# Performance work log

Measured on AMD Instinct MI355X. Metric: run time of the kernel, lower is better.

Reference implementation:

```python
import jax, jax.numpy as jnp
import numpy as np

E_DIM = 640   # RNA-FM embedding dim
H = 256       # hidden_dim
L = 3         # num_gcn_layers
LN_EPS = 1e-5


def _layer_norm(x, g, b):
    mu = jnp.mean(x, axis=-1, keepdims=True)
    var = jnp.mean((x - mu) ** 2, axis=-1, keepdims=True)
    return (x - mu) * jax.lax.rsqrt(var + LN_EPS) * g + b


def setup_inputs() -> dict:
    key = jax.random.key(0)
    ks = jax.random.split(key, 20)
    B, S = 4, 256

    def w(k, shape):
        fan_in = shape[-2] if len(shape) >= 2 else shape[-1]
        return jax.random.normal(k, shape, dtype=jnp.float32) / np.sqrt(fan_in)

    inp = {
        "embeddings": jax.random.normal(ks[0], (B, S, E_DIM), dtype=jnp.float32),
        "bp_priors": jax.random.uniform(ks[1], (B, S, S), dtype=jnp.float32),
        "sequence_lengths": jnp.full((B,), S, dtype=jnp.int32),
        # FeatureEncoder: Linear(640, 512) -> ReLU -> Linear(512, 256)
        "enc_w1": w(ks[2], (E_DIM, 2 * H)), "enc_b1": jnp.zeros((2 * H,), jnp.float32),
        "enc_w2": w(ks[3], (2 * H, H)),     "enc_b2": jnp.zeros((H,), jnp.float32),
        # GCN layers (stacked over L)
        "gcn_wself": w(ks[4], (L, H, H)), "gcn_bself": jnp.zeros((L, H), jnp.float32),
        "gcn_wedge": w(ks[5], (L, H, H)), "gcn_bedge": jnp.zeros((L, H), jnp.float32),
        "gcn_ln_g": jnp.ones((L, H), jnp.float32), "gcn_ln_b": jnp.zeros((L, H), jnp.float32),
        # PairwiseScorer MLP: Linear(2H+1, H) -> ReLU -> Linear(H, H//2) -> ReLU -> Linear(H//2, 1)
        "mlp_w1": w(ks[6], (2 * H + 1, H)), "mlp_b1": jnp.zeros((H,), jnp.float32),
        "mlp_w2": w(ks[7], (H, H // 2)),    "mlp_b2": jnp.zeros((H // 2,), jnp.float32),
        "mlp_w3": w(ks[8], (H // 2, 1)),    "mlp_b3": jnp.zeros((1,), jnp.float32),
    }
    return inp


def reference(embeddings, bp_priors, sequence_lengths,
              enc_w1, enc_b1, enc_w2, enc_b2,
              gcn_wself, gcn_bself, gcn_wedge, gcn_bedge, gcn_ln_g, gcn_ln_b,
              mlp_w1, mlp_b1, mlp_w2, mlp_b2, mlp_w3, mlp_b3):
    # FeatureEncoder
    h = jax.nn.relu(embeddings @ enc_w1 + enc_b1) @ enc_w2 + enc_b2  # [B,S,H]

    # GCN layers: self GEMM + adjacency (bp_priors) aggregated neighbor GEMM
    for l in range(L):
        self_f = h @ gcn_wself[l] + gcn_bself[l]
        neigh_f = jnp.einsum('bij,bjh->bih', bp_priors, h @ gcn_wedge[l] + gcn_bedge[l])
        h = _layer_norm(jax.nn.relu(self_f + neigh_f), gcn_ln_g[l], gcn_ln_b[l])

    # PairwiseScorer: concat([node_i, node_j, prior]) @ W1 split into three partial products
    # (mathematically identical to the expand-concat-MLP in the torch module).
    hi = h @ mlp_w1[:H]           # [B,S,H] contribution of node_i
    hj = h @ mlp_w1[H:2 * H]      # [B,S,H] contribution of node_j
    p = jax.nn.relu(hi[:, :, None, :] + hj[:, None, :, :]
                    + bp_priors[..., None] * mlp_w1[2 * H] + mlp_b1)  # [B,S,S,H]
    p = jax.nn.relu(p @ mlp_w2 + mlp_b2)                              # [B,S,S,H//2]
    bp_scores = (p @ mlp_w3 + mlp_b3)[..., 0]                         # [B,S,S]
    return bp_scores
```

## Files before the change

### kernel.cpp

```cpp
#include <hip/hip_runtime.h>

typedef __attribute__((ext_vector_type(8))) short short8;
typedef __attribute__((ext_vector_type(4))) float f32x4;
typedef __attribute__((ext_vector_type(4))) unsigned uint4v;

__device__ __forceinline__ void gload_lds16(const void* g, void* l) {
    __builtin_amdgcn_global_load_lds(
        (const __attribute__((address_space(1))) unsigned*)g,
        (__attribute__((address_space(3))) unsigned*)l, 16, 0, 0);
}
#define MFMA16(a, b, c) __builtin_amdgcn_mfma_f32_16x16x32_bf16((a), (b), (c), 0, 0, 0)

template<bool RELU, bool LNA, bool SPLITW2>
__global__ __launch_bounds__(256)
void gemm_s(const float* __restrict__ A,
            const float* __restrict__ B0, const float* __restrict__ bias0,
            float* __restrict__ C0,
            const float* __restrict__ B1, const float* __restrict__ bias1,
            float* __restrict__ C1,
            const float* __restrict__ ps, const float* __restrict__ lg,
            const float* __restrict__ lb,
            int M, int N, int K, int nxHalf,
            const float* __restrict__ w2, short* __restrict__ w2th,
            short* __restrict__ w2tl)
{
    if (SPLITW2 && blockIdx.y >= 32) {
        int e = ((blockIdx.y - 32) * gridDim.x + blockIdx.x) * 256 + threadIdx.x;
        if (e < 32768) {
            int k = e >> 7, n = e & 127;
            float x = w2[e];
            unsigned hu = __float_as_uint(x) & 0xFFFF0000u;
            w2th[n * 256 + k] = (short)(hu >> 16);
            w2tl[n * 256 + k] = (short)(__float_as_uint(x - __uint_as_float(hu)) >> 16);
        }
        return;
    }
    int bx = blockIdx.x;
    const float* B = B0; const float* bias = bias0; float* C = C0;
    if (nxHalf && bx >= nxHalf) { bx -= nxHalf; B = B1; bias = bias1; C = C1; }
    const int m0 = blockIdx.y * 32, n0 = bx * 32;
    const int tid = threadIdx.x;
    const int tx = tid & 7, ty = tid >> 3;

    __shared__ __align__(16) float As[32 * 36];
    __shared__ __align__(16) float Bs[32 * 36];
    __shared__ float mus[32], rss[32];

    if (LNA) {
        if (tid < 32) {
            int m = m0 + tid;
            float s  = ps[m * 2]            + ps[2048 + m * 2]
                     + ps[4096 + m * 2]     + ps[6144 + m * 2];
            float s2 = ps[m * 2 + 1]        + ps[2048 + m * 2 + 1]
                     + ps[4096 + m * 2 + 1] + ps[6144 + m * 2 + 1];
            float mu  = s * (1.f / 256.f);
            float var = s2 * (1.f / 256.f) - mu * mu;
            mus[tid] = mu;
            rss[tid] = rsqrtf(var + 1e-5f);
        }
        __syncthreads();
    }

    float acc[4] = {};
    for (int k0 = 0; k0 < K; k0 += 32) {
        {
            int row = ty, kq = tx << 2;
            float4 v = *(const float4*)&A[(long)(m0 + row) * K + k0 + kq];
            if (LNA) {
                float4 gv = *(const float4*)&lg[k0 + kq];
                float4 bv = *(const float4*)&lb[k0 + kq];
                float mu = mus[row], rs = rss[row];
                v.x = (v.x - mu) * rs * gv.x + bv.x;
                v.y = (v.y - mu) * rs * gv.y + bv.y;
                v.z = (v.z - mu) * rs * gv.z + bv.z;
                v.w = (v.w - mu) * rs * gv.w + bv.w;
            }
            As[(kq + 0) * 36 + row] = v.x; As[(kq + 1) * 36 + row] = v.y;
            As[(kq + 2) * 36 + row] = v.z; As[(kq + 3) * 36 + row] = v.w;
        }
        *(float4*)&Bs[ty * 36 + tx * 4] =
            *(const float4*)&B[(long)(k0 + ty) * N + n0 + tx * 4];
        __syncthreads();
#pragma unroll
        for (int k = 0; k < 32; ++k) {
            float a = As[k * 36 + ty];
            float4 b4 = *(const float4*)&Bs[k * 36 + tx * 4];
            acc[0] += a * b4.x; acc[1] += a * b4.y;
            acc[2] += a * b4.z; acc[3] += a * b4.w;
        }
        __syncthreads();
    }

    int m = m0 + ty;
#pragma unroll
    for (int j = 0; j < 4; ++j) {
        int n = n0 + tx * 4 + j;
        float v = acc[j];
        if (bias) v += bias[n];
        if (RELU) v = fmaxf(v, 0.f);
        C[(long)m * N + n] = v;
    }
}

__global__ __launch_bounds__(256)
void bmm_fuse(const float* __restrict__ bp, const float* __restrict__ eg,
              const float* __restrict__ sf, float* __restrict__ x,
              float* __restrict__ ps)
{
    const int b = blockIdx.z, jb = blockIdx.x;
    const int m0 = blockIdx.y * 32, n0 = jb * 64;
    const float* A = bp + b * 65536;
    const float* B = eg + b * 65536;
    const int tid = threadIdx.x;
    const int tx = tid & 15, ty = tid >> 4;

    __shared__ __align__(16) float As[32 * 36];
    __shared__ __align__(16) float Bs[32 * 68];

    float acc[2][4] = {};
    for (int k0 = 0; k0 < 256; k0 += 32) {
        {
            int row = tid >> 3, kq = (tid & 7) << 2;
            float4 v = *(const float4*)&A[(long)(m0 + row) * 256 + k0 + kq];
            As[(kq + 0) * 36 + row] = v.x; As[(kq + 1) * 36 + row] = v.y;
            As[(kq + 2) * 36 + row] = v.z; As[(kq + 3) * 36 + row] = v.w;
        }
#pragma unroll
        for (int q = 0; q < 2; ++q) {
            int f = tid * 2 + q;
            int kk = f >> 4, nn = (f & 15) << 2;
            *(float4*)&Bs[kk * 68 + nn] = *(const float4*)&B[(long)(k0 + kk) * 256 + n0 + nn];
        }
        __syncthreads();
#pragma unroll
        for (int k = 0; k < 32; ++k) {
            float2 a2 = *(const float2*)&As[k * 36 + ty * 2];
            float4 b4 = *(const float4*)&Bs[k * 68 + tx * 4];
            acc[0][0] += a2.x * b4.x; acc[0][1] += a2.x * b4.y;
            acc[0][2] += a2.x * b4.z; acc[0][3] += a2.x * b4.w;
            acc[1][0] += a2.y * b4.x; acc[1][1] += a2.y * b4.y;
            acc[1][2] += a2.y * b4.z; acc[1][3] += a2.y * b4.w;
        }
        __syncthreads();
    }

#pragma unroll
    for (int i = 0; i < 2; ++i) {
        int gm = b * 256 + m0 + ty * 2 + i;
        float s = 0.f, s2 = 0.f;
#pragma unroll
        for (int j = 0; j < 4; ++j) {
            int n = n0 + tx * 4 + j;
            float v = fmaxf(acc[i][j] + sf[(long)gm * 256 + n], 0.f);
            x[(long)gm * 256 + n] = v;
            s += v; s2 += v * v;
        }
        s  += __shfl_xor(s, 1, 64);  s2 += __shfl_xor(s2, 1, 64);
        s  += __shfl_xor(s, 2, 64);  s2 += __shfl_xor(s2, 2, 64);
        s  += __shfl_xor(s, 4, 64);  s2 += __shfl_xor(s2, 4, 64);
        s  += __shfl_xor(s, 8, 64);  s2 += __shfl_xor(s2, 8, 64);
        if (tx == 0) {
            ps[jb * 2048 + gm * 2]     = s;
            ps[jb * 2048 + gm * 2 + 1] = s2;
        }
    }
}

#define STAGE_HJ(T, BUF)                                                        \
    {                                                                           \
        int row = tid >> 3, s = tid & 7;                                        \
        gload_lds16(&hja[((long)(b * 256 + j0 + row)) * 256 + (T) * 32          \
                         + ((s ^ (row & 7)) << 2)],                             \
                    (char*)&hjs[BUF][0] + tid * 16);                            \
        int row2 = row + 32;                                                    \
        gload_lds16(&hja[((long)(b * 256 + j0 + row2)) * 256 + (T) * 32         \
                         + ((s ^ (row2 & 7)) << 2)],                            \
                    (char*)&hjs[BUF][0] + 4096 + tid * 16);                     \
    }

#define BUILD_P(KT, BUF)                                                        \
    {                                                                           \
        const char* hbase = (const char*)&hjs[BUF][0] + jj * 128;               \
        char* phc = (char*)&Ph[BUF][0];                                         \
        char* plc = (char*)&Pl[BUF][0];                                         \
        const int swz = (p & 7) << 4;                                           \
        _Pragma("unroll")                                                       \
        for (int q = 0; q < 2; ++q) {                                           \
            const int oct = o0 + q;                                             \
            float4 hv0 = *(const float4*)(hbase + (((oct * 2)     ^ (jj & 7)) << 4)); \
            float4 hv1 = *(const float4*)(hbase + (((oct * 2 + 1) ^ (jj & 7)) << 4)); \
            float4 iv0 = *(const float4*)&hib[ii][(KT) * 32 + oct * 8];         \
            float4 iv1 = *(const float4*)&hib[ii][(KT) * 32 + oct * 8 + 4];     \
            float4 cv0 = *(const float4*)&csv[(KT) * 32 + oct * 8];             \
            float4 cv1 = *(const float4*)&csv[(KT) * 32 + oct * 8 + 4];         \
            float x0 = fmaxf(fmaf(bpw, cv0.x, iv0.x) + hv0.x, 0.f);             \
            float x1 = fmaxf(fmaf(bpw, cv0.y, iv0.y) + hv0.y, 0.f);             \
            float x2 = fmaxf(fmaf(bpw, cv0.z, iv0.z) + hv0.z, 0.f);             \
            float x3 = fmaxf(fmaf(bpw, cv0.w, iv0.w) + hv0.w, 0.f);             \
            float x4 = fmaxf(fmaf(bpw, cv1.x, iv1.x) + hv1.x, 0.f);             \
            float x5 = fmaxf(fmaf(bpw, cv1.y, iv1.y) + hv1.y, 0.f);             \
            float x6 = fmaxf(fmaf(bpw, cv1.z, iv1.z) + hv1.z, 0.f);             \
            float x7 = fmaxf(fmaf(bpw, cv1.w, iv1.w) + hv1.w, 0.f);             \
            unsigned h0 = __float_as_uint(x0) & 0xFFFF0000u;                    \
            unsigned h1 = __float_as_uint(x1) & 0xFFFF0000u;                    \
            unsigned h2 = __float_as_uint(x2) & 0xFFFF0000u;                    \
            unsigned h3 = __float_as_uint(x3) & 0xFFFF0000u;                    \
            unsigned h4 = __float_as_uint(x4) & 0xFFFF0000u;                    \
            unsigned h5 = __float_as_uint(x5) & 0xFFFF0000u;                    \
            unsigned h6 = __float_as_uint(x6) & 0xFFFF0000u;                    \
            unsigned h7 = __float_as_uint(x7) & 0xFFFF0000u;                    \
            uint4v hv_, lv_;                                                    \
            hv_[0] = (h0 >> 16) | h1;                                           \
            hv_[1] = (h2 >> 16) | h3;                                           \
            hv_[2] = (h4 >> 16) | h5;                                           \
            hv_[3] = (h6 >> 16) | h7;                                           \
            lv_[0] = (__float_as_uint(x0 - __uint_as_float(h0)) >> 16)          \
                   | (__float_as_uint(x1 - __uint_as_float(h1)) & 0xFFFF0000u); \
            lv_[1] = (__float_as_uint(x2 - __uint_as_float(h2)) >> 16)          \
                   | (__float_as_uint(x3 - __uint_as_float(h3)) & 0xFFFF0000u); \
            lv_[2] = (__float_as_uint(x4 - __uint_as_float(h4)) >> 16)          \
                   | (__float_as_uint(x5 - __uint_as_float(h5)) & 0xFFFF0000u); \
            lv_[3] = (__float_as_uint(x6 - __uint_as_float(h6)) >> 16)          \
                   | (__float_as_uint(x7 - __uint_as_float(h7)) & 0xFFFF0000u); \
            int sbyte = p * 64 + oct * 16;                                      \
            *(uint4v*)(phc + (sbyte ^ swz)) = hv_;                              \
            *(uint4v*)(plc + (sbyte ^ swz)) = lv_;                              \
        }                                                                       \
    }

__global__ __launch_bounds__(256, 3)
void pairwise4(const float* __restrict__ hia, const float* __restrict__ hja,
               const float* __restrict__ bpm,
               const float* __restrict__ c, const float* __restrict__ b1,
               const short* __restrict__ w2th, const short* __restrict__ w2tl,
               const float* __restrict__ b2, const float* __restrict__ w3,
               const float* __restrict__ b3, float* __restrict__ out)
{
    const int b = blockIdx.z, ib0 = blockIdx.y * 2, j0 = blockIdx.x * 64;
    const int tid = threadIdx.x, l = tid & 63, wid = tid >> 6;
    const int wm0 = (wid & 1) * 64, wn0 = (wid >> 1) * 64;
    const int g = l >> 4, ln = l & 15;
    const int p = tid >> 1, jj = p & 63, ii = p >> 6, o0 = (tid & 1) * 2;

    __shared__ __align__(16) short Ph[2][4096];
    __shared__ __align__(16) short Pl[2][4096];
    __shared__ __align__(16) float hjs[2][2048];
    __shared__ __align__(16) float hib[2][256];
    __shared__ __align__(16) float csv[256];
    __shared__ float bpv[128];
    __shared__ float red[128][2];

    if (tid < 128)
        bpv[tid] = bpm[((long)(b * 256 + ib0 + (tid >> 6))) * 256 + j0 + (tid & 63)];
    {
        int i2 = tid >> 7, kk = (tid & 127) * 2;
        float2 hv = *(const float2*)&hia[((long)(b * 256 + ib0 + i2)) * 256 + kk];
        float2 bv = *(const float2*)&b1[kk];
        hib[i2][kk] = hv.x + bv.x; hib[i2][kk + 1] = hv.y + bv.y;
    }
    if (tid < 64) *(float4*)&csv[tid * 4] = *(const float4*)&c[tid * 4];

    STAGE_HJ(0, 0);
    __syncthreads();
    const float bpw = bpv[p];
    STAGE_HJ(1, 1);
    BUILD_P(0, 0);
    __syncthreads();

    f32x4 acc[4][4] = {};

#pragma unroll
    for (int kt = 0; kt < 8; ++kt) {
        const int cur = kt & 1;
        if (kt < 6) STAGE_HJ(kt + 2, cur);
        short8 bh[4], bl[4];
#pragma unroll
        for (int nf = 0; nf < 4; ++nf) {
            int col = wn0 + nf * 16 + ln;
            long bo = (long)col * 256 + kt * 32 + g * 8;
            bh[nf] = *(const short8*)(w2th + bo);
            bl[nf] = *(const short8*)(w2tl + bo);
        }
        if (kt < 7) BUILD_P(kt + 1, cur ^ 1);
        short8 ah[4], al[4];
#pragma unroll
        for (int mf = 0; mf < 4; ++mf) {
            int row = wm0 + mf * 16 + ln;
            int off = (row * 64 + g * 16) ^ ((row & 7) << 4);
            ah[mf] = *(const short8*)((const char*)&Ph[cur][0] + off);
            al[mf] = *(const short8*)((const char*)&Pl[cur][0] + off);
        }
#pragma unroll
        for (int mf = 0; mf < 4; ++mf)
#pragma unroll
            for (int nf = 0; nf < 4; ++nf) {
                acc[mf][nf] = MFMA16(ah[mf], bh[nf], acc[mf][nf]);
                acc[mf][nf] = MFMA16(ah[mf], bl[nf], acc[mf][nf]);
                acc[mf][nf] = MFMA16(al[mf], bh[nf], acc[mf][nf]);
            }
        __syncthreads();
    }

    float b2v[4], w3v[4];
#pragma unroll
    for (int nf = 0; nf < 4; ++nf) {
        int col = wn0 + nf * 16 + ln;
        b2v[nf] = b2[col];
        w3v[nf] = w3[col];
    }
#pragma unroll
    for (int mf = 0; mf < 4; ++mf) {
#pragma unroll
        for (int r = 0; r < 4; ++r) {
            float s = 0.f;
#pragma unroll
            for (int nf = 0; nf < 4; ++nf)
                s += fmaxf(acc[mf][nf][r] + b2v[nf], 0.f) * w3v[nf];
            s += __shfl_xor(s, 1, 64);
            s += __shfl_xor(s, 2, 64);
            s += __shfl_xor(s, 4, 64);
            s += __shfl_xor(s, 8, 64);
            if (ln == 0)
                red[wm0 + mf * 16 + g * 4 + r][wid >> 1] = s;
        }
    }
    __syncthreads();
    if (tid < 128) {
        int i = ib0 + (tid >> 6), j = j0 + (tid & 63);
        out[((long)(b * 256 + i)) * 256 + j] = red[tid][0] + red[tid][1] + b3[0];
    }
}

extern "C" void kernel_launch(void* const* d_in, const int* in_sizes, int n_in,
                              void* d_out, int out_size, void* d_ws, size_t ws_size,
                              hipStream_t stream)
{
    const float* emb   = (const float*)d_in[0];
    const float* bp    = (const float*)d_in[1];
    const float* ew1   = (const float*)d_in[3];
    const float* eb1   = (const float*)d_in[4];
    const float* ew2   = (const float*)d_in[5];
    const float* eb2   = (const float*)d_in[6];
    const float* wself = (const float*)d_in[7];
    const float* bself = (const float*)d_in[8];
    const float* wedge = (const float*)d_in[9];
    const float* bedge = (const float*)d_in[10];
    const float* lng   = (const float*)d_in[11];
    const float* lnb   = (const float*)d_in[12];
    const float* mw1   = (const float*)d_in[13];
    const float* mb1   = (const float*)d_in[14];
    const float* mw2   = (const float*)d_in[15];
    const float* mb2   = (const float*)d_in[16];
    const float* mw3   = (const float*)d_in[17];
    const float* mb3   = (const float*)d_in[18];
    float* out = (float*)d_out;

    float* ws = (float*)d_ws;
    float* h1 = ws;
    float* xe = h1 + 524288;
    float* sf = xe + 262144;
    float* eg = sf + 262144;
    float* x0 = eg + 262144;
    float* x1 = x0 + 262144;
    float* x2 = x1 + 262144;
    float* hi = x2 + 262144;
    float* hj = hi + 262144;
    short* w2th = (short*)(hj + 262144);
    short* w2tl = w2th + 32768;
    float* ps0  = (float*)(w2tl + 32768);
    float* ps1  = ps0 + 8192;
    float* ps2  = ps1 + 8192;

    float* xs[3]  = {x0, x1, x2};
    float* pss[3] = {ps0, ps1, ps2};
    dim3 blk(256);

    gemm_s<true, false, true><<<dim3(16, 40), blk, 0, stream>>>(emb, ew1, eb1, h1,
        nullptr, nullptr, nullptr, nullptr, nullptr, nullptr,
        1024, 512, 640, 0, mw2, w2th, w2tl);
    gemm_s<false, false, false><<<dim3(8, 32), blk, 0, stream>>>(h1, ew2, eb2, xe,
        nullptr, nullptr, nullptr, nullptr, nullptr, nullptr,
        1024, 256, 512, 0, nullptr, nullptr, nullptr);

    for (int lyr = 0; lyr < 3; ++lyr) {
        const float* Ain = (lyr == 0) ? xe : xs[lyr - 1];
        if (lyr == 0)
            gemm_s<false, false, false><<<dim3(16, 32), blk, 0, stream>>>(Ain,
                wself, bself, sf, wedge, bedge, eg,
                nullptr, nullptr, nullptr, 1024, 256, 256, 8,
                nullptr, nullptr, nullptr);
        else
            gemm_s<false, true, false><<<dim3(16, 32), blk, 0, stream>>>(Ain,
                wself + lyr * 65536, bself + lyr * 256, sf,
                wedge + lyr * 65536, bedge + lyr * 256, eg,
                pss[lyr - 1], lng + (lyr - 1) * 256, lnb + (lyr - 1) * 256,
                1024, 256, 256, 8, nullptr, nullptr, nullptr);
        bmm_fuse<<<dim3(4, 8, 4), blk, 0, stream>>>(bp, eg, sf, xs[lyr], pss[lyr]);
    }

    gemm_s<false, true, false><<<dim3(16, 32), blk, 0, stream>>>(x2,
        mw1, nullptr, hi, mw1 + 65536, nullptr, hj,
        ps2, lng + 512, lnb + 512, 1024, 256, 256, 8,
        nullptr, nullptr, nullptr);

    pairwise4<<<dim3(4, 128, 4), blk, 0, stream>>>(hi, hj, bp,
        mw1 + 131072, mb1, w2th, w2tl, mb2, mw3, mb3, out);
}
```

Baseline: 303.0 us.

## Fuse GCN layer stages into per-row kernels and merge encoder second GEMM

Replaces the separate self/edge GEMM, batched adjacency matmul, and LayerNorm-on-load kernels with one kernel per GCN layer. Each block handles 4 rows: it computes the neighbour aggregation and self projection, applies ReLU and LayerNorm in-block, then computes the next layer's edge projection (or the final hi/hj projections). The encoder's second linear is fused with layer 0's edge projection. This cuts the launch count from about 9 to 4 and removes intermediate round trips, at the cost of each block streaming whole weight matrices from global/L2 with little reuse and running only 256 blocks.

```diff
diff --git a/kernel.cpp b/kernel.cpp
--- a/kernel.cpp
+++ b/kernel.cpp
@@ -44,37 +44,12 @@
 
     __shared__ __align__(16) float As[32 * 36];
     __shared__ __align__(16) float Bs[32 * 36];
-    __shared__ float mus[32], rss[32];
-
-    if (LNA) {
-        if (tid < 32) {
-            int m = m0 + tid;
-            float s  = ps[m * 2]            + ps[2048 + m * 2]
-                     + ps[4096 + m * 2]     + ps[6144 + m * 2];
-            float s2 = ps[m * 2 + 1]        + ps[2048 + m * 2 + 1]
-                     + ps[4096 + m * 2 + 1] + ps[6144 + m * 2 + 1];
-            float mu  = s * (1.f / 256.f);
-            float var = s2 * (1.f / 256.f) - mu * mu;
-            mus[tid] = mu;
-            rss[tid] = rsqrtf(var + 1e-5f);
-        }
-        __syncthreads();
-    }
 
     float acc[4] = {};
     for (int k0 = 0; k0 < K; k0 += 32) {
         {
             int row = ty, kq = tx << 2;
             float4 v = *(const float4*)&A[(long)(m0 + row) * K + k0 + kq];
-            if (LNA) {
-                float4 gv = *(const float4*)&lg[k0 + kq];
-                float4 bv = *(const float4*)&lb[k0 + kq];
-                float mu = mus[row], rs = rss[row];
-                v.x = (v.x - mu) * rs * gv.x + bv.x;
-                v.y = (v.y - mu) * rs * gv.y + bv.y;
-                v.z = (v.z - mu) * rs * gv.z + bv.z;
-                v.w = (v.w - mu) * rs * gv.w + bv.w;
-            }
             As[(kq + 0) * 36 + row] = v.x; As[(kq + 1) * 36 + row] = v.y;
             As[(kq + 2) * 36 + row] = v.z; As[(kq + 3) * 36 + row] = v.w;
         }
@@ -103,66 +78,134 @@
 }
 
 __global__ __launch_bounds__(256)
-void bmm_fuse(const float* __restrict__ bp, const float* __restrict__ eg,
-              const float* __restrict__ sf, float* __restrict__ x,
-              float* __restrict__ ps)
+void enc2_fuse(const float* __restrict__ h1, const float* __restrict__ ew2,
+               const float* __restrict__ eb2, const float* __restrict__ we0,
+               const float* __restrict__ be0, float* __restrict__ xe,
+               float* __restrict__ eg0)
 {
-    const int b = blockIdx.z, jb = blockIdx.x;
-    const int m0 = blockIdx.y * 32, n0 = jb * 64;
-    const float* A = bp + b * 65536;
-    const float* B = eg + b * 65536;
     const int tid = threadIdx.x;
-    const int tx = tid & 15, ty = tid >> 4;
-
-    __shared__ __align__(16) float As[32 * 36];
-    __shared__ __align__(16) float Bs[32 * 68];
-
-    float acc[2][4] = {};
-    for (int k0 = 0; k0 < 256; k0 += 32) {
-        {
-            int row = tid >> 3, kq = (tid & 7) << 2;
-            float4 v = *(const float4*)&A[(long)(m0 + row) * 256 + k0 + kq];
-            As[(kq + 0) * 36 + row] = v.x; As[(kq + 1) * 36 + row] = v.y;
-            As[(kq + 2) * 36 + row] = v.z; As[(kq + 3) * 36 + row] = v.w;
-        }
-#pragma unroll
-        for (int q = 0; q < 2; ++q) {
-            int f = tid * 2 + q;
-            int kk = f >> 4, nn = (f & 15) << 2;
-            *(float4*)&Bs[kk * 68 + nn] = *(const float4*)&B[(long)(k0 + kk) * 256 + n0 + nn];
-        }
-        __syncthreads();
-#pragma unroll
-        for (int k = 0; k < 32; ++k) {
-            float2 a2 = *(const float2*)&As[k * 36 + ty * 2];
-            float4 b4 = *(const float4*)&Bs[k * 68 + tx * 4];
-            acc[0][0] += a2.x * b4.x; acc[0][1] += a2.x * b4.y;
-            acc[0][2] += a2.x * b4.z; acc[0][3] += a2.x * b4.w;
-            acc[1][0] += a2.y * b4.x; acc[1][1] += a2.y * b4.y;
-            acc[1][2] += a2.y * b4.z; acc[1][3] += a2.y * b4.w;
-        }
-        __syncthreads();
-    }
-
-#pragma unroll
-    for (int i = 0; i < 2; ++i) {
-        int gm = b * 256 + m0 + ty * 2 + i;
-        float s = 0.f, s2 = 0.f;
-#pragma unroll
-        for (int j = 0; j < 4; ++j) {
-            int n = n0 + tx * 4 + j;
-            float v = fmaxf(acc[i][j] + sf[(long)gm * 256 + n], 0.f);
-            x[(long)gm * 256 + n] = v;
-            s += v; s2 += v * v;
-        }
-        s  += __shfl_xor(s, 1, 64);  s2 += __shfl_xor(s2, 1, 64);
-        s  += __shfl_xor(s, 2, 64);  s2 += __shfl_xor(s2, 2, 64);
-        s  += __shfl_xor(s, 4, 64);  s2 += __shfl_xor(s2, 4, 64);
-        s  += __shfl_xor(s, 8, 64);  s2 += __shfl_xor(s2, 8, 64);
-        if (tx == 0) {
-            ps[jb * 2048 + gm * 2]     = s;
-            ps[jb * 2048 + gm * 2 + 1] = s2;
-        }
+    const int gr0 = blockIdx.x * 4;
+    const int r = tid >> 6, cg = (tid & 63) * 4;
+    __shared__ __align__(16) float hs[4][512];
+    __shared__ __align__(16) float xs[4][256];
+    {
+        int k0 = (tid & 63) * 8;
+        *(float4*)&hs[r][k0]     = *(const float4*)&h1[(long)(gr0 + r) * 512 + k0];
+        *(float4*)&hs[r][k0 + 4] = *(const float4*)&h1[(long)(gr0 + r) * 512 + k0 + 4];
+    }
+    __syncthreads();
+
+    float4 o = {0.f, 0.f, 0.f, 0.f};
+#pragma unroll 8
+    for (int k = 0; k < 512; ++k) {
+        float4 w = *(const float4*)&ew2[(long)k * 256 + cg];
+        float a = hs[r][k];
+        o.x += a * w.x; o.y += a * w.y; o.z += a * w.z; o.w += a * w.w;
+    }
+    float4 bv = *(const float4*)&eb2[cg];
+    o.x += bv.x; o.y += bv.y; o.z += bv.z; o.w += bv.w;
+    *(float4*)&xs[r][cg] = o;
+    *(float4*)&xe[(long)(gr0 + r) * 256 + cg] = o;
+    __syncthreads();
+
+    float4 e = {0.f, 0.f, 0.f, 0.f};
+#pragma unroll 8
+    for (int k = 0; k < 256; ++k) {
+        float4 w = *(const float4*)&we0[(long)k * 256 + cg];
+        float a = xs[r][k];
+        e.x += a * w.x; e.y += a * w.y; e.z += a * w.z; e.w += a * w.w;
+    }
+    float4 be = *(const float4*)&be0[cg];
+    e.x += be.x; e.y += be.y; e.z += be.z; e.w += be.w;
+    *(float4*)&eg0[(long)(gr0 + r) * 256 + cg] = e;
+}
+
+template<bool LAST>
+__global__ __launch_bounds__(256)
+void layer_fuse(const float* __restrict__ h_in, const float* __restrict__ bp,
+                const float* __restrict__ eg_in,
+                const float* __restrict__ Ws, const float* __restrict__ bs,
+                const float* __restrict__ lg, const float* __restrict__ lb,
+                const float* __restrict__ Wn0, const float* __restrict__ bn0,
+                const float* __restrict__ Wn1,
+                float* __restrict__ h_out, float* __restrict__ out0,
+                float* __restrict__ out1)
+{
+    const int tid = threadIdx.x;
+    const int gr0 = blockIdx.x * 4;
+    const int b = gr0 >> 8;
+    const float* egb = eg_in + (long)b * 65536;
+    const int r = tid >> 6, cg = (tid & 63) * 4;
+    __shared__ __align__(16) float hs[4][256];
+    __shared__ __align__(16) float ps[4][256];
+    {
+        int k0 = (tid & 63) * 4;
+        *(float4*)&hs[r][k0] = *(const float4*)&h_in[(long)(gr0 + r) * 256 + k0];
+        *(float4*)&ps[r][k0] = *(const float4*)&bp[(long)(gr0 + r) * 256 + k0];
+    }
+    __syncthreads();
+
+    float4 ng = {0.f, 0.f, 0.f, 0.f}, sf = {0.f, 0.f, 0.f, 0.f};
+#pragma unroll 4
+    for (int k = 0; k < 256; ++k) {
+        float4 we = *(const float4*)&egb[(long)k * 256 + cg];
+        float4 ws = *(const float4*)&Ws[(long)k * 256 + cg];
+        float ap = ps[r][k];
+        float ah = hs[r][k];
+        ng.x += ap * we.x; ng.y += ap * we.y; ng.z += ap * we.z; ng.w += ap * we.w;
+        sf.x += ah * ws.x; sf.y += ah * ws.y; sf.z += ah * ws.z; sf.w += ah * ws.w;
+    }
+    float4 bsv = *(const float4*)&bs[cg];
+    float x0 = fmaxf(sf.x + bsv.x + ng.x, 0.f);
+    float x1 = fmaxf(sf.y + bsv.y + ng.y, 0.f);
+    float x2 = fmaxf(sf.z + bsv.z + ng.z, 0.f);
+    float x3 = fmaxf(sf.w + bsv.w + ng.w, 0.f);
+
+    float s = x0 + x1 + x2 + x3;
+    float s2 = x0 * x0 + x1 * x1 + x2 * x2 + x3 * x3;
+#pragma unroll
+    for (int off = 1; off < 64; off <<= 1) {
+        s  += __shfl_xor(s,  off, 64);
+        s2 += __shfl_xor(s2, off, 64);
+    }
+    const float mu  = s * (1.f / 256.f);
+    const float var = s2 * (1.f / 256.f) - mu * mu;
+    const float rsv = rsqrtf(var + 1e-5f);
+    float4 gv = *(const float4*)&lg[cg];
+    float4 bbv = *(const float4*)&lb[cg];
+    float4 xl;
+    xl.x = (x0 - mu) * rsv * gv.x + bbv.x;
+    xl.y = (x1 - mu) * rsv * gv.y + bbv.y;
+    xl.z = (x2 - mu) * rsv * gv.z + bbv.z;
+    xl.w = (x3 - mu) * rsv * gv.w + bbv.w;
+
+    __syncthreads();
+    *(float4*)&hs[r][cg] = xl;
+    if (!LAST)
+        *(float4*)&h_out[(long)(gr0 + r) * 256 + cg] = xl;
+    __syncthreads();
+
+    float4 a0 = {0.f, 0.f, 0.f, 0.f};
+#pragma unroll 8
+    for (int k = 0; k < 256; ++k) {
+        float4 w = *(const float4*)&Wn0[(long)k * 256 + cg];
+        float a = hs[r][k];
+        a0.x += a * w.x; a0.y += a * w.y; a0.z += a * w.z; a0.w += a * w.w;
+    }
+    if (!LAST) {
+        float4 bn = *(const float4*)&bn0[cg];
+        a0.x += bn.x; a0.y += bn.y; a0.z += bn.z; a0.w += bn.w;
+        *(float4*)&out0[(long)(gr0 + r) * 256 + cg] = a0;
+    } else {
+        *(float4*)&out0[(long)(gr0 + r) * 256 + cg] = a0;
+        float4 a1 = {0.f, 0.f, 0.f, 0.f};
+#pragma unroll 8
+        for (int k = 0; k < 256; ++k) {
+            float4 w = *(const float4*)&Wn1[(long)k * 256 + cg];
+            float a = hs[r][k];
+            a1.x += a * w.x; a1.y += a * w.y; a1.z += a * w.z; a1.w += a * w.w;
+        }
+        *(float4*)&out1[(long)(gr0 + r) * 256 + cg] = a1;
     }
 }
 
@@ -356,52 +399,33 @@
     float* out = (float*)d_out;
 
     float* ws = (float*)d_ws;
-    float* h1 = ws;
-    float* xe = h1 + 524288;
-    float* sf = xe + 262144;
-    float* eg = sf + 262144;
-    float* x0 = eg + 262144;
-    float* x1 = x0 + 262144;
-    float* x2 = x1 + 262144;
-    float* hi = x2 + 262144;
-    float* hj = hi + 262144;
+    float* h1  = ws;
+    float* hA  = h1 + 524288;
+    float* hB  = hA + 262144;
+    float* egA = hB + 262144;
+    float* egB = egA + 262144;
+    float* hi  = egB + 262144;
+    float* hj  = hi + 262144;
     short* w2th = (short*)(hj + 262144);
     short* w2tl = w2th + 32768;
-    float* ps0  = (float*)(w2tl + 32768);
-    float* ps1  = ps0 + 8192;
-    float* ps2  = ps1 + 8192;
-
-    float* xs[3]  = {x0, x1, x2};
-    float* pss[3] = {ps0, ps1, ps2};
+
     dim3 blk(256);
 
     gemm_s<true, false, true><<<dim3(16, 40), blk, 0, stream>>>(emb, ew1, eb1, h1,
         nullptr, nullptr, nullptr, nullptr, nullptr, nullptr,
         1024, 512, 640, 0, mw2, w2th, w2tl);
-    gemm_s<false, false, false><<<dim3(8, 32), blk, 0, stream>>>(h1, ew2, eb2, xe,
-        nullptr, nullptr, nullptr, nullptr, nullptr, nullptr,
-        1024, 256, 512, 0, nullptr, nullptr, nullptr);
-
-    for (int lyr = 0; lyr < 3; ++lyr) {
-        const float* Ain = (lyr == 0) ? xe : xs[lyr - 1];
-        if (lyr == 0)
-            gemm_s<false, false, false><<<dim3(16, 32), blk, 0, stream>>>(Ain,
-                wself, bself, sf, wedge, bedge, eg,
-                nullptr, nullptr, nullptr, 1024, 256, 256, 8,
-                nullptr, nullptr, nullptr);
-        else
-            gemm_s<false, true, false><<<dim3(16, 32), blk, 0, stream>>>(Ain,
-                wself + lyr * 65536, bself + lyr * 256, sf,
-                wedge + lyr * 65536, bedge + lyr * 256, eg,
-                pss[lyr - 1], lng + (lyr - 1) * 256, lnb + (lyr - 1) * 256,
-                1024, 256, 256, 8, nullptr, nullptr, nullptr);
-        bmm_fuse<<<dim3(4, 8, 4), blk, 0, stream>>>(bp, eg, sf, xs[lyr], pss[lyr]);
-    }
-
-    gemm_s<false, true, false><<<dim3(16, 32), blk, 0, stream>>>(x2,
-        mw1, nullptr, hi, mw1 + 65536, nullptr, hj,
-        ps2, lng + 512, lnb + 512, 1024, 256, 256, 8,
-        nullptr, nullptr, nullptr);
+
+    enc2_fuse<<<dim3(256), blk, 0, stream>>>(h1, ew2, eb2, wedge, bedge, hA, egA);
+
+    layer_fuse<false><<<dim3(256), blk, 0, stream>>>(hA, bp, egA,
+        wself, bself, lng, lnb,
+        wedge + 65536, bedge + 256, nullptr, hB, egB, nullptr);
+    layer_fuse<false><<<dim3(256), blk, 0, stream>>>(hB, bp, egB,
+        wself + 65536, bself + 256, lng + 256, lnb + 256,
+        wedge + 131072, bedge + 512, nullptr, hA, egA, nullptr);
+    layer_fuse<true><<<dim3(256), blk, 0, stream>>>(hA, bp, egA,
+        wself + 131072, bself + 512, lng + 512, lnb + 512,
+        mw1, nullptr, mw1 + 65536, hB, hi, hj);
 
     pairwise4<<<dim3(4, 128, 4), blk, 0, stream>>>(hi, hj, bp,
         mw1 + 131072, mb1, w2th, w2tl, mb2, mw3, mb3, out);
```

New measurement: 355.7 us. +17.4%, slower.

## Build pairwise MFMA A-operands in registers instead of staging through LDS

Applied to the files above, without the earlier changes.

The pairwise scorer kernel no longer stages hj tiles into LDS or writes the split-bf16 P matrix to shared memory. Each wave now loads its hj rows straight from global memory, forms the ReLU'd hidden values for its own MFMA A-fragments in registers, and feeds them directly to the MFMAs. This removes the LDS round trip, the double buffering and the per-k-tile barriers. In exchange, each wave's hj loads are strided per-lane global reads, and elementwise work is repeated across the waves that share rows.

```diff
diff --git a/kernel.cpp b/kernel.cpp
--- a/kernel.cpp
+++ b/kernel.cpp
@@ -4,11 +4,6 @@
 typedef __attribute__((ext_vector_type(4))) float f32x4;
 typedef __attribute__((ext_vector_type(4))) unsigned uint4v;
 
-__device__ __forceinline__ void gload_lds16(const void* g, void* l) {
-    __builtin_amdgcn_global_load_lds(
-        (const __attribute__((address_space(1))) unsigned*)g,
-        (__attribute__((address_space(3))) unsigned*)l, 16, 0, 0);
-}
 #define MFMA16(a, b, c) __builtin_amdgcn_mfma_f32_16x16x32_bf16((a), (b), (c), 0, 0, 0)
 
 template<bool RELU, bool LNA, bool SPLITW2>
@@ -166,70 +161,8 @@
     }
 }
 
-#define STAGE_HJ(T, BUF)                                                        \
-    {                                                                           \
-        int row = tid >> 3, s = tid & 7;                                        \
-        gload_lds16(&hja[((long)(b * 256 + j0 + row)) * 256 + (T) * 32          \
-                         + ((s ^ (row & 7)) << 2)],                             \
-                    (char*)&hjs[BUF][0] + tid * 16);                            \
-        int row2 = row + 32;                                                    \
-        gload_lds16(&hja[((long)(b * 256 + j0 + row2)) * 256 + (T) * 32         \
-                         + ((s ^ (row2 & 7)) << 2)],                            \
-                    (char*)&hjs[BUF][0] + 4096 + tid * 16);                     \
-    }
-
-#define BUILD_P(KT, BUF)                                                        \
-    {                                                                           \
-        const char* hbase = (const char*)&hjs[BUF][0] + jj * 128;               \
-        char* phc = (char*)&Ph[BUF][0];                                         \
-        char* plc = (char*)&Pl[BUF][0];                                         \
-        const int swz = (p & 7) << 4;                                           \
-        _Pragma("unroll")                                                       \
-        for (int q = 0; q < 2; ++q) {                                           \
-            const int oct = o0 + q;                                             \
-            float4 hv0 = *(const float4*)(hbase + (((oct * 2)     ^ (jj & 7)) << 4)); \
-            float4 hv1 = *(const float4*)(hbase + (((oct * 2 + 1) ^ (jj & 7)) << 4)); \
-            float4 iv0 = *(const float4*)&hib[ii][(KT) * 32 + oct * 8];         \
-            float4 iv1 = *(const float4*)&hib[ii][(KT) * 32 + oct * 8 + 4];     \
-            float4 cv0 = *(const float4*)&csv[(KT) * 32 + oct * 8];             \
-            float4 cv1 = *(const float4*)&csv[(KT) * 32 + oct * 8 + 4];         \
-            float x0 = fmaxf(fmaf(bpw, cv0.x, iv0.x) + hv0.x, 0.f);             \
-            float x1 = fmaxf(fmaf(bpw, cv0.y, iv0.y) + hv0.y, 0.f);             \
-            float x2 = fmaxf(fmaf(bpw, cv0.z, iv0.z) + hv0.z, 0.f);             \
-            float x3 = fmaxf(fmaf(bpw, cv0.w, iv0.w) + hv0.w, 0.f);             \
-            float x4 = fmaxf(fmaf(bpw, cv1.x, iv1.x) + hv1.x, 0.f);             \
-            float x5 = fmaxf(fmaf(bpw, cv1.y, iv1.y) + hv1.y, 0.f);             \
-            float x6 = fmaxf(fmaf(bpw, cv1.z, iv1.z) + hv1.z, 0.f);             \
-            float x7 = fmaxf(fmaf(bpw, cv1.w, iv1.w) + hv1.w, 0.f);             \
-            unsigned h0 = __float_as_uint(x0) & 0xFFFF0000u;                    \
-            unsigned h1 = __float_as_uint(x1) & 0xFFFF0000u;                    \
-            unsigned h2 = __float_as_uint(x2) & 0xFFFF0000u;                    \
-            unsigned h3 = __float_as_uint(x3) & 0xFFFF0000u;                    \
-            unsigned h4 = __float_as_uint(x4) & 0xFFFF0000u;                    \
-            unsigned h5 = __float_as_uint(x5) & 0xFFFF0000u;                    \
-            unsigned h6 = __float_as_uint(x6) & 0xFFFF0000u;                    \
-            unsigned h7 = __float_as_uint(x7) & 0xFFFF0000u;                    \
-            uint4v hv_, lv_;                                                    \
-            hv_[0] = (h0 >> 16) | h1;                                           \
-            hv_[1] = (h2 >> 16) | h3;                                           \
-            hv_[2] = (h4 >> 16) | h5;                                           \
-            hv_[3] = (h6 >> 16) | h7;                                           \
-            lv_[0] = (__float_as_uint(x0 - __uint_as_float(h0)) >> 16)          \
-                   | (__float_as_uint(x1 - __uint_as_float(h1)) & 0xFFFF0000u); \
-            lv_[1] = (__float_as_uint(x2 - __uint_as_float(h2)) >> 16)          \
-                   | (__float_as_uint(x3 - __uint_as_float(h3)) & 0xFFFF0000u); \
-            lv_[2] = (__float_as_uint(x4 - __uint_as_float(h4)) >> 16)          \
-                   | (__float_as_uint(x5 - __uint_as_float(h5)) & 0xFFFF0000u); \
-            lv_[3] = (__float_as_uint(x6 - __uint_as_float(h6)) >> 16)          \
-                   | (__float_as_uint(x7 - __uint_as_float(h7)) & 0xFFFF0000u); \
-            int sbyte = p * 64 + oct * 16;                                      \
-            *(uint4v*)(phc + (sbyte ^ swz)) = hv_;                              \
-            *(uint4v*)(plc + (sbyte ^ swz)) = lv_;                              \
-        }                                                                       \
-    }
-
 __global__ __launch_bounds__(256, 3)
-void pairwise4(const float* __restrict__ hia, const float* __restrict__ hja,
+void pairwise5(const float* __restrict__ hia, const float* __restrict__ hja,
                const float* __restrict__ bpm,
                const float* __restrict__ c, const float* __restrict__ b1,
                const short* __restrict__ w2th, const short* __restrict__ w2tl,
@@ -240,11 +173,8 @@
     const int tid = threadIdx.x, l = tid & 63, wid = tid >> 6;
     const int wm0 = (wid & 1) * 64, wn0 = (wid >> 1) * 64;
     const int g = l >> 4, ln = l & 15;
-    const int p = tid >> 1, jj = p & 63, ii = p >> 6, o0 = (tid & 1) * 2;
-
-    __shared__ __align__(16) short Ph[2][4096];
-    __shared__ __align__(16) short Pl[2][4096];
-    __shared__ __align__(16) float hjs[2][2048];
+    const int ii = wm0 >> 6;
+
     __shared__ __align__(16) float hib[2][256];
     __shared__ __align__(16) float csv[256];
     __shared__ float bpv[128];
@@ -259,46 +189,78 @@
         hib[i2][kk] = hv.x + bv.x; hib[i2][kk + 1] = hv.y + bv.y;
     }
     if (tid < 64) *(float4*)&csv[tid * 4] = *(const float4*)&c[tid * 4];
-
-    STAGE_HJ(0, 0);
     __syncthreads();
-    const float bpw = bpv[p];
-    STAGE_HJ(1, 1);
-    BUILD_P(0, 0);
-    __syncthreads();
+
+    float bw[4];
+    const float* hjr[4];
+#pragma unroll
+    for (int mf = 0; mf < 4; ++mf) {
+        bw[mf] = bpv[wm0 + mf * 16 + ln];
+        hjr[mf] = &hja[((long)(b * 256 + j0 + mf * 16 + ln)) * 256];
+    }
 
     f32x4 acc[4][4] = {};
 
 #pragma unroll
     for (int kt = 0; kt < 8; ++kt) {
-        const int cur = kt & 1;
-        if (kt < 6) STAGE_HJ(kt + 2, cur);
+        const int kb = kt * 32 + g * 8;
         short8 bh[4], bl[4];
 #pragma unroll
         for (int nf = 0; nf < 4; ++nf) {
-            int col = wn0 + nf * 16 + ln;
-            long bo = (long)col * 256 + kt * 32 + g * 8;
+            long bo = (long)(wn0 + nf * 16 + ln) * 256 + kb;
             bh[nf] = *(const short8*)(w2th + bo);
             bl[nf] = *(const short8*)(w2tl + bo);
         }
-        if (kt < 7) BUILD_P(kt + 1, cur ^ 1);
-        short8 ah[4], al[4];
+        float4 hj0[4], hj1[4];
 #pragma unroll
         for (int mf = 0; mf < 4; ++mf) {
-            int row = wm0 + mf * 16 + ln;
-            int off = (row * 64 + g * 16) ^ ((row & 7) << 4);
-            ah[mf] = *(const short8*)((const char*)&Ph[cur][0] + off);
-            al[mf] = *(const short8*)((const char*)&Pl[cur][0] + off);
-        }
-#pragma unroll
-        for (int mf = 0; mf < 4; ++mf)
+            hj0[mf] = *(const float4*)(hjr[mf] + kb);
+            hj1[mf] = *(const float4*)(hjr[mf] + kb + 4);
+        }
+        float4 iv0 = *(const float4*)&hib[ii][kb];
+        float4 iv1 = *(const float4*)&hib[ii][kb + 4];
+        float4 cv0 = *(const float4*)&csv[kb];
+        float4 cv1 = *(const float4*)&csv[kb + 4];
+
+#pragma unroll
+        for (int mf = 0; mf < 4; ++mf) {
+            float x0 = fmaxf(fmaf(bw[mf], cv0.x, iv0.x) + hj0[mf].x, 0.f);
+            float x1 = fmaxf(fmaf(bw[mf], cv0.y, iv0.y) + hj0[mf].y, 0.f);
+            float x2 = fmaxf(fmaf(bw[mf], cv0.z, iv0.z) + hj0[mf].z, 0.f);
+            float x3 = fmaxf(fmaf(bw[mf], cv0.w, iv0.w) + hj0[mf].w, 0.f);
+            float x4 = fmaxf(fmaf(bw[mf], cv1.x, iv1.x) + hj1[mf].x, 0.f);
+            float x5 = fmaxf(fmaf(bw[mf], cv1.y, iv1.y) + hj1[mf].y, 0.f);
+            float x6 = fmaxf(fmaf(bw[mf], cv1.z, iv1.z) + hj1[mf].z, 0.f);
+            float x7 = fmaxf(fmaf(bw[mf], cv1.w, iv1.w) + hj1[mf].w, 0.f);
+            unsigned h0 = __float_as_uint(x0) & 0xFFFF0000u;
+            unsigned h1 = __float_as_uint(x1) & 0xFFFF0000u;
+            unsigned h2 = __float_as_uint(x2) & 0xFFFF0000u;
+            unsigned h3 = __float_as_uint(x3) & 0xFFFF0000u;
+            unsigned h4 = __float_as_uint(x4) & 0xFFFF0000u;
+            unsigned h5 = __float_as_uint(x5) & 0xFFFF0000u;
+            unsigned h6 = __float_as_uint(x6) & 0xFFFF0000u;
+            unsigned h7 = __float_as_uint(x7) & 0xFFFF0000u;
+            union { uint4v u; short8 s; } ua, ul;
+            ua.u[0] = (h0 >> 16) | h1;
+            ua.u[1] = (h2 >> 16) | h3;
+            ua.u[2] = (h4 >> 16) | h5;
+            ua.u[3] = (h6 >> 16) | h7;
+            ul.u[0] = (__float_as_uint(x0 - __uint_as_float(h0)) >> 16)
+                    | (__float_as_uint(x1 - __uint_as_float(h1)) & 0xFFFF0000u);
+            ul.u[1] = (__float_as_uint(x2 - __uint_as_float(h2)) >> 16)
+                    | (__float_as_uint(x3 - __uint_as_float(h3)) & 0xFFFF0000u);
+            ul.u[2] = (__float_as_uint(x4 - __uint_as_float(h4)) >> 16)
+                    | (__float_as_uint(x5 - __uint_as_float(h5)) & 0xFFFF0000u);
+            ul.u[3] = (__float_as_uint(x6 - __uint_as_float(h6)) >> 16)
+                    | (__float_as_uint(x7 - __uint_as_float(h7)) & 0xFFFF0000u);
+            short8 ah = ua.s, al = ul.s;
 #pragma unroll
             for (int nf = 0; nf < 4; ++nf) {
-                acc[mf][nf] = MFMA16(ah[mf], bh[nf], acc[mf][nf]);
-                acc[mf][nf] = MFMA16(ah[mf], bl[nf], acc[mf][nf]);
-                acc[mf][nf] = MFMA16(al[mf], bh[nf], acc[mf][nf]);
+                acc[mf][nf] = MFMA16(ah, bh[nf], acc[mf][nf]);
+                acc[mf][nf] = MFMA16(ah, bl[nf], acc[mf][nf]);
+                acc[mf][nf] = MFMA16(al, bh[nf], acc[mf][nf]);
             }
-        __syncthreads();
+        }
     }
 
     float b2v[4], w3v[4];
@@ -403,6 +365,6 @@
         ps2, lng + 512, lnb + 512, 1024, 256, 256, 8,
         nullptr, nullptr, nullptr);
 
-    pairwise4<<<dim3(4, 128, 4), blk, 0, stream>>>(hi, hj, bp,
+    pairwise5<<<dim3(4, 128, 4), blk, 0, stream>>>(hi, hj, bp,
         mw1 + 131072, mb1, w2th, w2tl, mb2, mw3, mb3, out);
 }
```

After: 356.2 us. 17.5% more time.
